# Performance work log

Measured on AMD Instinct MI355X. Metric: run time of the kernel, lower is better.

The kernel has to match this reference:

```python
import jax, jax.numpy as jnp
import numpy as np


def _hungarian(a):
    """Jonker-Volgenant / Kuhn-Munkres shortest-augmenting-path LAP solver.
    a: (n, n) float numpy cost matrix. Returns col_ind (int64, len n) such that
    row i is matched to column col_ind[i] (row_ind is implicitly arange(n),
    exactly like scipy.optimize.linear_sum_assignment on a square matrix).
    """
    n = a.shape[0]
    INF = np.inf
    u = np.zeros(n + 1)
    v = np.zeros(n + 1)
    p = np.zeros(n + 1, dtype=np.int64)   # p[j] = row currently matched to column j
    way = np.zeros(n + 1, dtype=np.int64)
    for i in range(1, n + 1):
        p[0] = i
        j0 = 0
        minv = np.full(n + 1, INF)
        used = np.zeros(n + 1, dtype=bool)
        while True:
            used[j0] = True
            i0 = p[j0]
            cur = a[i0 - 1] - u[i0] - v[1:]          # reduced costs of row i0
            free = ~used[1:]
            better = free & (cur < minv[1:])
            minv[1:] = np.where(better, cur, minv[1:])
            way[1:] = np.where(better, j0, way[1:])
            cand = np.where(free, minv[1:], INF)
            j1 = int(np.argmin(cand)) + 1
            delta = cand[j1 - 1]
            u[p[used]] += delta
            v[used] -= delta
            minv[1:] = np.where(free, minv[1:] - delta, minv[1:])
            j0 = j1
            if p[j0] == 0:
                break
        while j0 != 0:                               # augment along alternating path
            j1 = int(way[j0])
            p[j0] = p[j1]
            j0 = j1
    col_ind = np.zeros(n, dtype=np.int64)
    col_ind[p[1:] - 1] = np.arange(n)
    return col_ind


def _matching(input, target):
    sx = jnp.sum(input * input, axis=-1)
    sy = jnp.sum(target * target, axis=-1)
    cost = sx[:, :, None] + sy[:, None, :] - 2.0 * jnp.einsum('bkd,bmd->bkm', input, target)
    cost_np = np.asarray(jax.device_get(cost), dtype=np.float64)
    perms = np.stack([_hungarian(c) for c in cost_np])  # (B, k)
    return jnp.asarray(perms)


def setup_inputs() -> dict:
    key = jax.random.key(0)
    k1, k2 = jax.random.split(key)
    B, K, D = 512, 128, 512
    return {
        "input": jax.random.normal(k1, (B, K, D), dtype=jnp.float32),
        "target": jax.random.normal(k2, (B, K, D), dtype=jnp.float32),
    }


def reference(input, target):
    # Hungarian assignment is computed on detached costs (constant wrt grads).
    perms = _matching(input, target)                       # (B, k)
    matched_target = jnp.take_along_axis(target, perms[:, :, None], axis=1)
    # Per-batch mean over (k, d), then mean over batch == global mean (equal sizes).
    return jnp.mean((input - matched_target) ** 2)
```

## Files before the change

kernel.cpp:

```cpp
#include <hip/hip_runtime.h>
#include <hip/hip_bf16.h>

#define K_PTS 128
#define DIM   512
#define BK    32
#define XS_STRIDE 132

__device__ __forceinline__ int rdlane_i(int v, int lane) {
    return __builtin_amdgcn_readlane(v, lane);
}
__device__ __forceinline__ float rdlane_f(float v, int lane) {
    return __int_as_float(__builtin_amdgcn_readlane(__float_as_int(v), lane));
}
__device__ __forceinline__ void wave_fence() {
    asm volatile("s_waitcnt lgkmcnt(0)" ::: "memory");
}

#define DPP_ID 0xFFFFFFFFu

template <int CTRL, int RM>
__device__ __forceinline__ unsigned dpp_min1(unsigned k) {
    unsigned o = (unsigned)__builtin_amdgcn_update_dpp((int)DPP_ID, (int)k, CTRL, RM, 0xF, false);
    return min(k, o);
}
__device__ __forceinline__ unsigned wave_min_u32(unsigned k) {
    k = dpp_min1<0x111, 0xF>(k);
    k = dpp_min1<0x112, 0xF>(k);
    k = dpp_min1<0x114, 0xF>(k);
    k = dpp_min1<0x118, 0xF>(k);
    k = dpp_min1<0x142, 0xA>(k);
    k = dpp_min1<0x143, 0xC>(k);
    return (unsigned)rdlane_i((int)k, 63);
}
template <int CTRL, int RM>
__device__ __forceinline__ void dpp_min2(unsigned& best, unsigned& sec) {
    unsigned ob = (unsigned)__builtin_amdgcn_update_dpp((int)DPP_ID, (int)best, CTRL, RM, 0xF, false);
    unsigned os = (unsigned)__builtin_amdgcn_update_dpp((int)DPP_ID, (int)sec,  CTRL, RM, 0xF, false);
    sec  = min(max(best, ob), min(sec, os));
    best = min(best, ob);
}
__device__ __forceinline__ void wave_min2_u32(unsigned& best, unsigned& sec) {
    dpp_min2<0x111, 0xF>(best, sec);
    dpp_min2<0x112, 0xF>(best, sec);
    dpp_min2<0x114, 0xF>(best, sec);
    dpp_min2<0x118, 0xF>(best, sec);
    dpp_min2<0x142, 0xA>(best, sec);
    dpp_min2<0x143, 0xC>(best, sec);
    best = (unsigned)rdlane_i((int)best, 63);
    sec  = (unsigned)rdlane_i((int)sec, 63);
}

__global__ __launch_bounds__(256, 2)
void hungarian_mse_kernel(const float* __restrict__ X, const float* __restrict__ Y,
                          float* __restrict__ out, float inv_total) {
    const int b = blockIdx.x;
    const int t = threadIdx.x;

    __shared__ float A[K_PTS * K_PTS];
    __shared__ float sx_sh[K_PTS];
    __shared__ float sy_sh[K_PTS];
    __shared__ float u_sh[K_PTS];
    __shared__ int   rmatch[K_PTS];
    __shared__ int   wl[512];
    __shared__ int   wl_n;

    float* Xs = A;
    float* Ys = A + BK * XS_STRIDE;

    const float* Xg = X + (size_t)b * K_PTS * DIM;
    const float* Yg = Y + (size_t)b * K_PTS * DIM;

    float acc[8][8];
#pragma unroll
    for (int i = 0; i < 8; ++i)
#pragma unroll
        for (int j = 0; j < 8; ++j) acc[i][j] = 0.0f;

    float nrm = 0.0f;
    const int tx = t & 15;
    const int ty = t >> 4;

    for (int k0 = 0; k0 < DIM; k0 += BK) {
        __syncthreads();
#pragma unroll
        for (int i = 0; i < 4; ++i) {
            int idx = t + i * 256;
            int r  = idx >> 3;
            int kq = idx & 7;
            float4 vx = *(const float4*)(Xg + r * DIM + k0 + kq * 4);
            float4 vy = *(const float4*)(Yg + r * DIM + k0 + kq * 4);
            int kb = kq * 4;
            Xs[(kb + 0) * XS_STRIDE + r] = vx.x;
            Xs[(kb + 1) * XS_STRIDE + r] = vx.y;
            Xs[(kb + 2) * XS_STRIDE + r] = vx.z;
            Xs[(kb + 3) * XS_STRIDE + r] = vx.w;
            Ys[(kb + 0) * XS_STRIDE + r] = vy.x;
            Ys[(kb + 1) * XS_STRIDE + r] = vy.y;
            Ys[(kb + 2) * XS_STRIDE + r] = vy.z;
            Ys[(kb + 3) * XS_STRIDE + r] = vy.w;
        }
        __syncthreads();
        for (int kk = 0; kk < BK; ++kk) {
            const float* xrow = Xs + kk * XS_STRIDE;
            const float* yrow = Ys + kk * XS_STRIDE;
            float4 xa = *(const float4*)(xrow + ty * 8);
            float4 xb = *(const float4*)(xrow + ty * 8 + 4);
            float4 ya = *(const float4*)(yrow + tx * 8);
            float4 yb = *(const float4*)(yrow + tx * 8 + 4);
            float av[8] = {xa.x, xa.y, xa.z, xa.w, xb.x, xb.y, xb.z, xb.w};
            float bv[8] = {ya.x, ya.y, ya.z, ya.w, yb.x, yb.y, yb.z, yb.w};
#pragma unroll
            for (int i = 0; i < 8; ++i)
#pragma unroll
                for (int j = 0; j < 8; ++j)
                    acc[i][j] = fmaf(av[i], bv[j], acc[i][j]);
        }
        if (t < 128) {
#pragma unroll
            for (int kk = 0; kk < BK; ++kk) {
                float v = Xs[kk * XS_STRIDE + t];
                nrm = fmaf(v, v, nrm);
            }
        } else {
#pragma unroll
            for (int kk = 0; kk < BK; ++kk) {
                float v = Ys[kk * XS_STRIDE + (t - 128)];
                nrm = fmaf(v, v, nrm);
            }
        }
    }
    if (t < 128) sx_sh[t] = nrm; else sy_sh[t - 128] = nrm;
    if (t < 128) u_sh[t] = 0.0f;
    __syncthreads();
#pragma unroll
    for (int i = 0; i < 8; ++i) {
        int r = ty * 8 + i;
        float sxr = sx_sh[r];
#pragma unroll
        for (int j = 0; j < 8; ++j) {
            int c = tx * 8 + j;
            A[r * K_PTS + c] = sxr + sy_sh[c] - 2.0f * acc[i][j];
        }
    }
    __syncthreads();

    if (t < 64) {
        asm volatile("s_setprio 3");
        float v0, v1;
        int p_lo = -1, p_hi = -1;

        rmatch[t] = -1; rmatch[t + 64] = -1;
        wave_fence();
        {
            float m0 = 1e30f, m1 = 1e30f;
            int a0 = 0, a1 = 0;
#pragma unroll 4
            for (int i = 0; i < K_PTS; ++i) {
                float c0 = A[i * K_PTS + t];
                float c1 = A[i * K_PTS + 64 + t];
                if (c0 < m0) { m0 = c0; a0 = i; }
                if (c1 < m1) { m1 = c1; a1 = i; }
            }
            v0 = m0; v1 = m1;
            int w0 = atomicCAS(&rmatch[a0], -1, (int)t);
            if (w0 == -1) p_lo = a0;
            int w1 = atomicCAS(&rmatch[a1], -1, (int)(t + 64));
            if (w1 == -1) p_hi = a1;
        }
        wave_fence();

        sy_sh[t] = v0; sy_sh[t + 64] = v1;
        wave_fence();
#pragma unroll
        for (int which = 0; which < 2; ++which) {
            int i  = t + which * 64;
            int j1 = rmatch[i];
            float mu = 1e30f;
            if (j1 >= 0) {
#pragma unroll 4
                for (int s = 0; s < K_PTS; ++s) {
                    int jj = (s + t) & 127;
                    float rc = A[i * K_PTS + jj] - sy_sh[jj];
                    if (jj != j1) mu = fminf(mu, rc);
                }
            }
            sx_sh[i] = mu;
        }
        wave_fence();
        if (p_lo >= 0) { float mu = sx_sh[p_lo]; v0 = A[p_lo * K_PTS + t]      - mu; u_sh[p_lo] = mu; }
        if (p_hi >= 0) { float mu = sx_sh[p_hi]; v1 = A[p_hi * K_PTS + 64 + t] - mu; u_sh[p_hi] = mu; }
        wave_fence();

        if (t == 0) {
            int n = 0;
            for (int i = 0; i < K_PTS; ++i) if (rmatch[i] < 0) wl[n++] = i;
            wl_n = n;
        }
        wave_fence();

        {
            int head = 0, tail = wl_n, steps = 0;
            while (head < tail && steps < 320) {
                ++steps;
                int i = wl[head++];
                float r0 = fmaxf(A[i * K_PTS + t]      - v0, 0.0f);
                float r1 = fmaxf(A[i * K_PTS + 64 + t] - v1, 0.0f);
                unsigned k0 = (__float_as_uint(r0) & 0xFFFFFF80u) | (unsigned)t;
                unsigned k1 = (__float_as_uint(r1) & 0xFFFFFF80u) | (unsigned)(t + 64);
                unsigned best = min(k0, k1), sec = max(k0, k1);
                wave_min2_u32(best, sec);
                int j1 = (int)(best & 127u);
                int j2 = (int)(sec & 127u);
                float mu = rdlane_f((j1 >= 64) ? r1 : r0, j1 & 63);
                float nu = rdlane_f((j2 >= 64) ? r1 : r0, j2 & 63);
                if (t == 0) u_sh[i] = nu;
                int kO = rdlane_i((j1 >= 64) ? p_hi : p_lo, j1 & 63);
                bool strict = (mu < nu);
                if (strict && t == (j1 & 63)) {
                    float d = nu - mu;
                    if (j1 >= 64) v1 -= d; else v0 -= d;
                }
                int jA = j1;
                if (!strict && kO >= 0) {
                    int k2 = rdlane_i((j2 >= 64) ? p_hi : p_lo, j2 & 63);
                    if (k2 < 0) jA = j2;
                }
                int kOld = rdlane_i((jA >= 64) ? p_hi : p_lo, jA & 63);
                if (t == (jA & 63)) { if (jA >= 64) p_hi = i; else p_lo = i; }
                if (t == 0) {
                    rmatch[i] = jA;
                    if (kOld >= 0) { rmatch[kOld] = -1; wl[tail] = kOld; }
                }
                if (kOld >= 0) ++tail;
                wave_fence();
            }
        }

        if (t == 0) {
            int n = 0;
            for (int i = 0; i < K_PTS; ++i) if (rmatch[i] < 0) wl[n++] = i;
            wl_n = n;
        }
        wave_fence();
        const int nfree = wl_n;

        for (int idx = 0; idx < nfree; ++idx) {
            int row = wl[idx];
            float u_i = u_sh[row];
            float dist0 = fmaxf(A[row * K_PTS + t]      - u_i - v0, 0.0f);
            float dist1 = fmaxf(A[row * K_PTS + 64 + t] - u_i - v1, 0.0f);
            int way0 = 128, way1 = 128;
            bool sc0 = false, sc1 = false;
            int j1 = 0;
            float D = 0.0f;

            while (true) {
                unsigned k0 = sc0 ? 0xFFFFFFFFu
                                  : ((__float_as_uint(dist0) & 0xFFFFFF80u) | (unsigned)t);
                unsigned k1 = sc1 ? 0xFFFFFFFFu
                                  : ((__float_as_uint(dist1) & 0xFFFFFF80u) | (unsigned)(t + 64));
                unsigned k = wave_min_u32(min(k0, k1));
                j1 = (int)(k & 127u);
                int lane = j1 & 63;
                bool hi = j1 >= 64;
                D       = rdlane_f(hi ? dist1 : dist0, lane);
                int i1  = rdlane_i(hi ? p_hi : p_lo, lane);
                if (i1 < 0) break;

                if (j1 == t)      sc0 = true;
                if (j1 == t + 64) sc1 = true;

                float ui1 = u_sh[i1];
                float a0 = A[i1 * K_PTS + t];
                float a1 = A[i1 * K_PTS + 64 + t];
                float base = D - ui1;
                if (!sc0) {
                    float c0 = fmaxf((a0 - v0) + base, 0.0f);
                    if (c0 < dist0) { dist0 = c0; way0 = j1; }
                }
                if (!sc1) {
                    float c1 = fmaxf((a1 - v1) + base, 0.0f);
                    if (c1 < dist1) { dist1 = c1; way1 = j1; }
                }
            }

            if (sc0) { float del = D - dist0; v0 -= del; u_sh[p_lo] += del; }
            if (sc1) { float del = D - dist1; v1 -= del; u_sh[p_hi] += del; }
            if (t == 0) u_sh[row] += D;

            int j0 = j1;
            while (true) {
                int lane0 = j0 & 63;
                bool hi0 = j0 >= 64;
                int jp = rdlane_i(hi0 ? way1 : way0, lane0);
                int pv;
                if (jp == 128) pv = row;
                else           pv = rdlane_i((jp >= 64) ? p_hi : p_lo, jp & 63);
                if (!hi0 && j0 == t)      p_lo = pv;
                if ( hi0 && j0 == t + 64) p_hi = pv;
                if (jp == 128) break;
                j0 = jp;
            }
            wave_fence();
        }

        float tsum = A[p_lo * K_PTS + t] + A[p_hi * K_PTS + 64 + t];
#pragma unroll
        for (int m = 1; m <= 32; m <<= 1)
            tsum += __shfl_xor(tsum, m, 64);
        if (t == 0) atomicAdd(out, tsum * inv_total);
    }
}

extern "C" void kernel_launch(void* const* d_in, const int* in_sizes, int n_in,
                              void* d_out, int out_size, void* d_ws, size_t ws_size,
                              hipStream_t stream) {
    const float* X = (const float*)d_in[0];
    const float* Y = (const float*)d_in[1];
    float* out = (float*)d_out;

    const int total = in_sizes[0];
    const int B = total / (K_PTS * DIM);
    const float inv_total = 1.0f / (float)total;

    hipMemsetAsync(out, 0, out_size * sizeof(float), stream);
    hungarian_mse_kernel<<<dim3(B), dim3(256), 0, stream>>>(X, Y, out, inv_total);
}
```

Baseline: 688.0 us.

## Interleave column ownership per lane and vectorize LDS cost accesses

Each lane now owns adjacent columns 2t and 2t+1 instead of t and t+64, so row reads from the shared cost matrix become single float2 loads. Reduced costs are decoded straight from the packed min key instead of readlanes, and row potentials are read via readlane from registers cached at the start of each augmentation, replacing LDS reads. The cost-matrix write-out uses float4 stores. The goal is fewer LDS instructions and cross-lane ops on the serial Hungarian critical path. The cached u registers could go stale if u_sh changes inside the Dijkstra loop, but it is only updated after it.

```diff
diff --git a/kernel.cpp b/kernel.cpp
--- a/kernel.cpp
+++ b/kernel.cpp
@@ -136,16 +136,23 @@
     for (int i = 0; i < 8; ++i) {
         int r = ty * 8 + i;
         float sxr = sx_sh[r];
-#pragma unroll
-        for (int j = 0; j < 8; ++j) {
-            int c = tx * 8 + j;
-            A[r * K_PTS + c] = sxr + sy_sh[c] - 2.0f * acc[i][j];
-        }
+        float4 o0, o1;
+        o0.x = sxr + sy_sh[tx * 8 + 0] - 2.0f * acc[i][0];
+        o0.y = sxr + sy_sh[tx * 8 + 1] - 2.0f * acc[i][1];
+        o0.z = sxr + sy_sh[tx * 8 + 2] - 2.0f * acc[i][2];
+        o0.w = sxr + sy_sh[tx * 8 + 3] - 2.0f * acc[i][3];
+        o1.x = sxr + sy_sh[tx * 8 + 4] - 2.0f * acc[i][4];
+        o1.y = sxr + sy_sh[tx * 8 + 5] - 2.0f * acc[i][5];
+        o1.z = sxr + sy_sh[tx * 8 + 6] - 2.0f * acc[i][6];
+        o1.w = sxr + sy_sh[tx * 8 + 7] - 2.0f * acc[i][7];
+        *(float4*)&A[r * K_PTS + tx * 8]     = o0;
+        *(float4*)&A[r * K_PTS + tx * 8 + 4] = o1;
     }
     __syncthreads();
 
     if (t < 64) {
         asm volatile("s_setprio 3");
+        const int c0 = 2 * t, c1 = 2 * t + 1;
         float v0, v1;
         int p_lo = -1, p_hi = -1;
 
@@ -156,20 +163,19 @@
             int a0 = 0, a1 = 0;
 #pragma unroll 4
             for (int i = 0; i < K_PTS; ++i) {
-                float c0 = A[i * K_PTS + t];
-                float c1 = A[i * K_PTS + 64 + t];
-                if (c0 < m0) { m0 = c0; a0 = i; }
-                if (c1 < m1) { m1 = c1; a1 = i; }
+                float2 cc = *(const float2*)&A[i * K_PTS + c0];
+                if (cc.x < m0) { m0 = cc.x; a0 = i; }
+                if (cc.y < m1) { m1 = cc.y; a1 = i; }
             }
             v0 = m0; v1 = m1;
-            int w0 = atomicCAS(&rmatch[a0], -1, (int)t);
+            int w0 = atomicCAS(&rmatch[a0], -1, c0);
             if (w0 == -1) p_lo = a0;
-            int w1 = atomicCAS(&rmatch[a1], -1, (int)(t + 64));
+            int w1 = atomicCAS(&rmatch[a1], -1, c1);
             if (w1 == -1) p_hi = a1;
         }
         wave_fence();
 
-        sy_sh[t] = v0; sy_sh[t + 64] = v1;
+        *(float2*)&sy_sh[c0] = make_float2(v0, v1);
         wave_fence();
 #pragma unroll
         for (int which = 0; which < 2; ++which) {
@@ -178,17 +184,21 @@
             float mu = 1e30f;
             if (j1 >= 0) {
 #pragma unroll 4
-                for (int s = 0; s < K_PTS; ++s) {
-                    int jj = (s + t) & 127;
-                    float rc = A[i * K_PTS + jj] - sy_sh[jj];
-                    if (jj != j1) mu = fminf(mu, rc);
+                for (int s = 0; s < 64; ++s) {
+                    int jj = (s + t) & 63;
+                    float2 cc = *(const float2*)&A[i * K_PTS + 2 * jj];
+                    float2 vv = *(const float2*)&sy_sh[2 * jj];
+                    float r0 = cc.x - vv.x;
+                    float r1 = cc.y - vv.y;
+                    if (2 * jj     != j1) mu = fminf(mu, r0);
+                    if (2 * jj + 1 != j1) mu = fminf(mu, r1);
                 }
             }
             sx_sh[i] = mu;
         }
         wave_fence();
-        if (p_lo >= 0) { float mu = sx_sh[p_lo]; v0 = A[p_lo * K_PTS + t]      - mu; u_sh[p_lo] = mu; }
-        if (p_hi >= 0) { float mu = sx_sh[p_hi]; v1 = A[p_hi * K_PTS + 64 + t] - mu; u_sh[p_hi] = mu; }
+        if (p_lo >= 0) { float mu = sx_sh[p_lo]; v0 = A[p_lo * K_PTS + c0] - mu; u_sh[p_lo] = mu; }
+        if (p_hi >= 0) { float mu = sx_sh[p_hi]; v1 = A[p_hi * K_PTS + c1] - mu; u_sh[p_hi] = mu; }
         wave_fence();
 
         if (t == 0) {
@@ -203,30 +213,31 @@
             while (head < tail && steps < 320) {
                 ++steps;
                 int i = wl[head++];
-                float r0 = fmaxf(A[i * K_PTS + t]      - v0, 0.0f);
-                float r1 = fmaxf(A[i * K_PTS + 64 + t] - v1, 0.0f);
-                unsigned k0 = (__float_as_uint(r0) & 0xFFFFFF80u) | (unsigned)t;
-                unsigned k1 = (__float_as_uint(r1) & 0xFFFFFF80u) | (unsigned)(t + 64);
+                float2 cc = *(const float2*)&A[i * K_PTS + c0];
+                float r0 = fmaxf(cc.x - v0, 0.0f);
+                float r1 = fmaxf(cc.y - v1, 0.0f);
+                unsigned k0 = (__float_as_uint(r0) & 0xFFFFFF80u) | (unsigned)c0;
+                unsigned k1 = (__float_as_uint(r1) & 0xFFFFFF80u) | (unsigned)c1;
                 unsigned best = min(k0, k1), sec = max(k0, k1);
                 wave_min2_u32(best, sec);
                 int j1 = (int)(best & 127u);
                 int j2 = (int)(sec & 127u);
-                float mu = rdlane_f((j1 >= 64) ? r1 : r0, j1 & 63);
-                float nu = rdlane_f((j2 >= 64) ? r1 : r0, j2 & 63);
+                float mu = __uint_as_float(best & 0xFFFFFF80u);
+                float nu = __uint_as_float(sec  & 0xFFFFFF80u);
                 if (t == 0) u_sh[i] = nu;
-                int kO = rdlane_i((j1 >= 64) ? p_hi : p_lo, j1 & 63);
+                int kO = rdlane_i((j1 & 1) ? p_hi : p_lo, j1 >> 1);
                 bool strict = (mu < nu);
-                if (strict && t == (j1 & 63)) {
+                if (strict && t == (j1 >> 1)) {
                     float d = nu - mu;
-                    if (j1 >= 64) v1 -= d; else v0 -= d;
+                    if (j1 & 1) v1 -= d; else v0 -= d;
                 }
                 int jA = j1;
                 if (!strict && kO >= 0) {
-                    int k2 = rdlane_i((j2 >= 64) ? p_hi : p_lo, j2 & 63);
+                    int k2 = rdlane_i((j2 & 1) ? p_hi : p_lo, j2 >> 1);
                     if (k2 < 0) jA = j2;
                 }
-                int kOld = rdlane_i((jA >= 64) ? p_hi : p_lo, jA & 63);
-                if (t == (jA & 63)) { if (jA >= 64) p_hi = i; else p_lo = i; }
+                int kOld = rdlane_i((jA & 1) ? p_hi : p_lo, jA >> 1);
+                if (t == (jA >> 1)) { if (jA & 1) p_hi = i; else p_lo = i; }
                 if (t == 0) {
                     rmatch[i] = jA;
                     if (kOld >= 0) { rmatch[kOld] = -1; wl[tail] = kOld; }
@@ -246,9 +257,12 @@
 
         for (int idx = 0; idx < nfree; ++idx) {
             int row = wl[idx];
-            float u_i = u_sh[row];
-            float dist0 = fmaxf(A[row * K_PTS + t]      - u_i - v0, 0.0f);
-            float dist1 = fmaxf(A[row * K_PTS + 64 + t] - u_i - v1, 0.0f);
+            float u_lo_reg = u_sh[t];
+            float u_hi_reg = u_sh[t + 64];
+            float u_row = rdlane_f((row >= 64) ? u_hi_reg : u_lo_reg, row & 63);
+            float2 rc = *(const float2*)&A[row * K_PTS + c0];
+            float dist0 = fmaxf(rc.x - u_row - v0, 0.0f);
+            float dist1 = fmaxf(rc.y - u_row - v1, 0.0f);
             int way0 = 128, way1 = 128;
             bool sc0 = false, sc1 = false;
             int j1 = 0;
@@ -256,31 +270,28 @@
 
             while (true) {
                 unsigned k0 = sc0 ? 0xFFFFFFFFu
-                                  : ((__float_as_uint(dist0) & 0xFFFFFF80u) | (unsigned)t);
+                                  : ((__float_as_uint(dist0) & 0xFFFFFF80u) | (unsigned)c0);
                 unsigned k1 = sc1 ? 0xFFFFFFFFu
-                                  : ((__float_as_uint(dist1) & 0xFFFFFF80u) | (unsigned)(t + 64));
+                                  : ((__float_as_uint(dist1) & 0xFFFFFF80u) | (unsigned)c1);
                 unsigned k = wave_min_u32(min(k0, k1));
                 j1 = (int)(k & 127u);
-                int lane = j1 & 63;
-                bool hi = j1 >= 64;
-                D       = rdlane_f(hi ? dist1 : dist0, lane);
-                int i1  = rdlane_i(hi ? p_hi : p_lo, lane);
+                D  = __uint_as_float(k & 0xFFFFFF80u);
+                int i1 = rdlane_i((j1 & 1) ? p_hi : p_lo, j1 >> 1);
                 if (i1 < 0) break;
 
-                if (j1 == t)      sc0 = true;
-                if (j1 == t + 64) sc1 = true;
-
-                float ui1 = u_sh[i1];
-                float a0 = A[i1 * K_PTS + t];
-                float a1 = A[i1 * K_PTS + 64 + t];
-                float base = D - ui1;
+                if (j1 == c0) sc0 = true;
+                if (j1 == c1) sc1 = true;
+
+                float u_i1 = rdlane_f((i1 >= 64) ? u_hi_reg : u_lo_reg, i1 & 63);
+                float2 aa = *(const float2*)&A[i1 * K_PTS + c0];
+                float base = D - u_i1;
                 if (!sc0) {
-                    float c0 = fmaxf((a0 - v0) + base, 0.0f);
-                    if (c0 < dist0) { dist0 = c0; way0 = j1; }
+                    float cv = fmaxf((aa.x - v0) + base, 0.0f);
+                    if (cv < dist0) { dist0 = cv; way0 = j1; }
                 }
                 if (!sc1) {
-                    float c1 = fmaxf((a1 - v1) + base, 0.0f);
-                    if (c1 < dist1) { dist1 = c1; way1 = j1; }
+                    float cv = fmaxf((aa.y - v1) + base, 0.0f);
+                    if (cv < dist1) { dist1 = cv; way1 = j1; }
                 }
             }
 
@@ -290,21 +301,21 @@
 
             int j0 = j1;
             while (true) {
-                int lane0 = j0 & 63;
-                bool hi0 = j0 >= 64;
-                int jp = rdlane_i(hi0 ? way1 : way0, lane0);
+                int lane0 = j0 >> 1;
+                bool odd = (j0 & 1) != 0;
+                int jp = rdlane_i(odd ? way1 : way0, lane0);
                 int pv;
                 if (jp == 128) pv = row;
-                else           pv = rdlane_i((jp >= 64) ? p_hi : p_lo, jp & 63);
-                if (!hi0 && j0 == t)      p_lo = pv;
-                if ( hi0 && j0 == t + 64) p_hi = pv;
+                else           pv = rdlane_i((jp & 1) ? p_hi : p_lo, jp >> 1);
+                if (!odd && lane0 == t) p_lo = pv;
+                if ( odd && lane0 == t) p_hi = pv;
                 if (jp == 128) break;
                 j0 = jp;
             }
             wave_fence();
         }
 
-        float tsum = A[p_lo * K_PTS + t] + A[p_hi * K_PTS + 64 + t];
+        float tsum = A[p_lo * K_PTS + c0] + A[p_hi * K_PTS + c1];
 #pragma unroll
         for (int m = 1; m <= 32; m <<= 1)
             tsum += __shfl_xor(tsum, m, 64);
```

Measured after the change: 680.6 us. Within noise of the previous version (-1.1%).
